# Kernel optimization log

Measured on AMD Instinct MI355X. Metric: run time of the kernel, lower is better.

Reference implementation:

```python
import jax, jax.numpy as jnp
import numpy as np

B, C, H, W = 4, 256, 64, 64
C8 = C // 8


def setup_inputs() -> dict:
    key = jax.random.key(0)
    ks = jax.random.split(key, 8)
    x = jax.random.normal(ks[0], (B, C, H, W), dtype=jnp.float32)
    # 1x1 conv weights act as per-pixel linear maps: [out_ch, in_ch]
    Wq = jax.random.normal(ks[1], (C8, C), dtype=jnp.float32) * 0.05
    bq = jax.random.normal(ks[2], (C8,), dtype=jnp.float32) * 0.01
    Wk = jax.random.normal(ks[3], (C8, C), dtype=jnp.float32) * 0.05
    bk = jax.random.normal(ks[4], (C8,), dtype=jnp.float32) * 0.01
    Wv = jax.random.normal(ks[5], (C, C), dtype=jnp.float32) * 0.05
    bv = jax.random.normal(ks[6], (C,), dtype=jnp.float32) * 0.01
    # torch inits gamma to 0 (identity); use nonzero so output exercises the attention path
    gamma = jnp.array(0.5, dtype=jnp.float32)
    return {"x": x, "Wq": Wq, "bq": bq, "Wk": Wk, "bk": bk, "Wv": Wv, "bv": bv, "gamma": gamma}


def reference(x, Wq, bq, Wk, bk, Wv, bv, gamma):
    b, c, h, w = x.shape
    n = h * w
    xf = x.reshape(b, c, n)                                   # [B,C,N]
    q = jnp.einsum('oc,bcn->bno', Wq, xf) + bq                # [B,N,C8] (proj_query permuted)
    k = jnp.einsum('oc,bcn->bon', Wk, xf) + bk[:, None]       # [B,C8,N]
    energy = jnp.einsum('bnc,bcm->bnm', q, k)                 # [B,N_q,N_k]
    # NOTE: torch Softmax(dim=1) -> normalize over the QUERY axis (axis=1)
    attention = jax.nn.softmax(energy, axis=1)
    v = jnp.einsum('oc,bcn->bon', Wv, xf) + bv[:, None]       # [B,C,N]
    out = jnp.einsum('bcn,bnm->bcm', v, attention).reshape(b, c, h, w)
    return gamma * out + x
```

## Files before the change

kernel.cpp:

```cpp
#include <hip/hip_runtime.h>
#include <hip/hip_bf16.h>

#define BN 4
#define CC 256
#define C8 32
#define NN 4096
#define PROJ_ROWS 320
#define LOG2E 1.4426950408889634f

typedef __attribute__((ext_vector_type(8))) short short8;
typedef __attribute__((ext_vector_type(4))) float f32x4;

__device__ __forceinline__ unsigned short f2bf(float f) {
    unsigned u = __builtin_bit_cast(unsigned, f);
    unsigned r = (u + 0x7fffu + ((u >> 16) & 1u)) >> 16;
    return (unsigned short)r;
}
__device__ __forceinline__ float bfhi2f(unsigned u) { return __builtin_bit_cast(float, u & 0xffff0000u); }
__device__ __forceinline__ float bflo2f(unsigned u) { return __builtin_bit_cast(float, u << 16); }

__global__ __launch_bounds__(256) void proj_kernel(
    const float* __restrict__ x,
    const float* __restrict__ Wq, const float* __restrict__ bq,
    const float* __restrict__ Wk, const float* __restrict__ bk,
    const float* __restrict__ Wv, const float* __restrict__ bv,
    unsigned short* __restrict__ proj, unsigned short* __restrict__ qT)
{
    int bid = blockIdx.x;
    int b = bid >> 7, nt = bid & 127;
    int n0 = nt * 32;
    int tid = threadIdx.x;
    int w = tid >> 6, l = tid & 63, l15 = l & 15, lq = l >> 4;

    __shared__ alignas(16) unsigned short Xt[32][264];

    int c_l = tid >> 3;
    int nb  = (tid & 7) * 4;

#pragma unroll
    for (int kc = 0; kc < 8; kc++) {
        const float* xp = x + ((size_t)(b * CC + kc * 32 + c_l)) * NN + n0 + nb;
        float4 x0 = *(const float4*)xp;
        Xt[nb + 0][kc * 32 + c_l] = f2bf(x0.x);
        Xt[nb + 1][kc * 32 + c_l] = f2bf(x0.y);
        Xt[nb + 2][kc * 32 + c_l] = f2bf(x0.z);
        Xt[nb + 3][kc * 32 + c_l] = f2bf(x0.w);
    }
    __syncthreads();

    f32x4 acc[5][2];
#pragma unroll
    for (int gi = 0; gi < 5; gi++)
#pragma unroll
        for (int mi = 0; mi < 2; mi++) acc[gi][mi] = (f32x4){0.f, 0.f, 0.f, 0.f};

    for (int kc = 0; kc < 8; kc++) {
        float4 wf[5][2];
#pragma unroll
        for (int gi = 0; gi < 5; gi++) {
            int og = (w * 5 + gi) * 16 + l15;
            const float* wrow = (og < 32) ? (Wq + (size_t)og * CC)
                              : (og < 64) ? (Wk + (size_t)(og - 32) * CC)
                                          : (Wv + (size_t)(og - 64) * CC);
            const float* wp = wrow + kc * 32 + lq * 8;
            wf[gi][0] = *(const float4*)wp;
            wf[gi][1] = *(const float4*)(wp + 4);
        }
#pragma unroll
        for (int gi = 0; gi < 5; gi++) {
            unsigned short a8[8] __attribute__((aligned(16)));
            float tw[8] = {wf[gi][0].x, wf[gi][0].y, wf[gi][0].z, wf[gi][0].w,
                           wf[gi][1].x, wf[gi][1].y, wf[gi][1].z, wf[gi][1].w};
#pragma unroll
            for (int e = 0; e < 8; e++) a8[e] = f2bf(tw[e]);
            short8 af = *(const short8*)a8;
#pragma unroll
            for (int mi = 0; mi < 2; mi++) {
                short8 bf = *(const short8*)&Xt[mi * 16 + l15][kc * 32 + lq * 8];
                acc[gi][mi] = __builtin_amdgcn_mfma_f32_16x16x32_bf16(af, bf, acc[gi][mi], 0, 0, 0);
            }
        }
    }

#pragma unroll
    for (int gi = 0; gi < 5; gi++) {
#pragma unroll
        for (int r = 0; r < 4; r++) {
            int og = (w * 5 + gi) * 16 + lq * 4 + r;
            float bias = (og < 32) ? bq[og] : (og < 64) ? bk[og - 32] : bv[og - 64];
            bool is_k = (og >= 32) && (og < 64);
#pragma unroll
            for (int mi = 0; mi < 2; mi++) {
                int n = n0 + mi * 16 + l15;
                float v = acc[gi][mi][r] + bias;
                if (is_k) v *= LOG2E;
                unsigned short v16 = f2bf(v);
                if (og < 32) {
                    qT[((size_t)b * NN + n) * C8 + og] = v16;
                } else {
                    proj[((size_t)b * PROJ_ROWS + og) * NN + n] = v16;
                }
            }
        }
    }
}

template<int NSPLIT, bool FINAL>
__global__ __launch_bounds__(256, 4) void attn_kernel(
    const unsigned short* __restrict__ proj,
    const unsigned short* __restrict__ qT,
    const float* __restrict__ x,
    const float* __restrict__ gamma_p,
    float* __restrict__ out,
    unsigned short* __restrict__ Opart,
    float* __restrict__ Lpart)
{
    constexpr int ITERS = 64 / NSPLIT;
    int bid = blockIdx.x;
    int low = bid & 255;
    int xcd = low & 7;
    int b = xcd >> 1;
    int mtile = ((low >> 3) << 1) | (xcd & 1);
    int m0 = mtile * 64;
    int ch = (bid >> 8) & 1;
    int h  = bid >> 9;
    int nbase = h * (ITERS * 64);

    int tid = threadIdx.x;
    int w = tid >> 6, l = tid & 63, l15 = l & 15, lq = l >> 4;
    int cw = ch * 128 + w * 32;

    __shared__ alignas(16) unsigned short ps[2][64][72];
    __shared__ float red[4][64];
    __shared__ float Ltot[64];

    const unsigned short* kbase = proj + ((size_t)b * PROJ_ROWS + C8) * NN;
    const unsigned short* vbase = proj + ((size_t)b * PROJ_ROWS + 64) * NN;
    const unsigned short* qbase = qT + (size_t)b * NN * C8;

    short8 kfrag[4];
#pragma unroll
    for (int mi = 0; mi < 4; mi++) {
        int col = m0 + mi * 16 + l15;
        unsigned short t8[8] __attribute__((aligned(16)));
#pragma unroll
        for (int j = 0; j < 8; j++)
            t8[j] = kbase[(size_t)(lq * 8 + j) * NN + col];
        kfrag[mi] = *(const short8*)t8;
    }

    f32x4 O[2][4];
#pragma unroll
    for (int ci = 0; ci < 2; ci++)
#pragma unroll
        for (int mi = 0; mi < 4; mi++) O[ci][mi] = (f32x4){0.f, 0.f, 0.f, 0.f};
    float runS[4] = {0.f, 0.f, 0.f, 0.f};

    short8 avc[2][2];
#pragma unroll
    for (int kh = 0; kh < 2; kh++)
#pragma unroll
        for (int ci = 0; ci < 2; ci++)
            avc[kh][ci] = *(const short8*)(vbase
                + (size_t)(cw + ci * 16 + l15) * NN + nbase + kh * 32 + lq * 8);
    {
        short8 qf = *(const short8*)(qbase + (size_t)(nbase + 16 * w + l15) * C8 + lq * 8);
#pragma unroll
        for (int mi = 0; mi < 4; mi++) {
            f32x4 S = __builtin_amdgcn_mfma_f32_16x16x32_bf16(
                qf, kfrag[mi], (f32x4){0.f, 0.f, 0.f, 0.f}, 0, 0, 0);
            float p0 = exp2f(S[0]), p1 = exp2f(S[1]), p2 = exp2f(S[2]), p3 = exp2f(S[3]);
            runS[mi] += (p0 + p1) + (p2 + p3);
            unsigned pk0 = (unsigned)f2bf(p0) | ((unsigned)f2bf(p1) << 16);
            unsigned pk1 = (unsigned)f2bf(p2) | ((unsigned)f2bf(p3) << 16);
            *(uint2*)&ps[0][mi * 16 + l15][16 * w + lq * 4] = make_uint2(pk0, pk1);
        }
    }

    for (int it = 0; it < ITERS; it++) {
        int n0c = nbase + it * 64;
        __syncthreads();

        short8 avn[2][2];
        short8 qn;
        if (it + 1 < ITERS) {
            int nn = n0c + 64;
#pragma unroll
            for (int kh = 0; kh < 2; kh++)
#pragma unroll
                for (int ci = 0; ci < 2; ci++)
                    avn[kh][ci] = *(const short8*)(vbase
                        + (size_t)(cw + ci * 16 + l15) * NN + nn + kh * 32 + lq * 8);
            qn = *(const short8*)(qbase + (size_t)(nn + 16 * w + l15) * C8 + lq * 8);
        }

        const unsigned short* psrc = &ps[it & 1][0][0];
#pragma unroll
        for (int kh = 0; kh < 2; kh++) {
            short8 bfr[4];
#pragma unroll
            for (int mi = 0; mi < 4; mi++)
                bfr[mi] = *(const short8*)(psrc + (mi * 16 + l15) * 72 + kh * 32 + lq * 8);
#pragma unroll
            for (int ci = 0; ci < 2; ci++)
#pragma unroll
                for (int mi = 0; mi < 4; mi++)
                    O[ci][mi] = __builtin_amdgcn_mfma_f32_16x16x32_bf16(
                        avc[kh][ci], bfr[mi], O[ci][mi], 0, 0, 0);
        }

        if (it + 1 < ITERS) {
#pragma unroll
            for (int mi = 0; mi < 4; mi++) {
                f32x4 S = __builtin_amdgcn_mfma_f32_16x16x32_bf16(
                    qn, kfrag[mi], (f32x4){0.f, 0.f, 0.f, 0.f}, 0, 0, 0);
                float p0 = exp2f(S[0]), p1 = exp2f(S[1]), p2 = exp2f(S[2]), p3 = exp2f(S[3]);
                runS[mi] += (p0 + p1) + (p2 + p3);
                unsigned pk0 = (unsigned)f2bf(p0) | ((unsigned)f2bf(p1) << 16);
                unsigned pk1 = (unsigned)f2bf(p2) | ((unsigned)f2bf(p3) << 16);
                *(uint2*)(&ps[(it + 1) & 1][0][0] + (mi * 16 + l15) * 72 + 16 * w + lq * 4)
                    = make_uint2(pk0, pk1);
            }
#pragma unroll
            for (int kh = 0; kh < 2; kh++)
#pragma unroll
                for (int ci = 0; ci < 2; ci++) avc[kh][ci] = avn[kh][ci];
        }
    }

#pragma unroll
    for (int mi = 0; mi < 4; mi++) {
        float s = runS[mi];
        s += __shfl_xor(s, 16);
        s += __shfl_xor(s, 32);
        red[w][mi * 16 + l15] = s;
    }
    __syncthreads();
    if (tid < 64) Ltot[tid] = red[0][tid] + red[1][tid] + red[2][tid] + red[3][tid];
    __syncthreads();

    if constexpr (FINAL) {
        float gamma = gamma_p[0];
        float iv[4];
#pragma unroll
        for (int mi = 0; mi < 4; mi++) iv[mi] = 1.0f / Ltot[mi * 16 + l15];
#pragma unroll
        for (int ci = 0; ci < 2; ci++) {
#pragma unroll
            for (int mi = 0; mi < 4; mi++) {
                int m = m0 + mi * 16 + l15;
#pragma unroll
                for (int r = 0; r < 4; r++) {
                    int c = cw + ci * 16 + lq * 4 + r;
                    size_t idx = ((size_t)b * CC + c) * NN + m;
                    out[idx] = gamma * (O[ci][mi][r] * iv[mi]) + x[idx];
                }
            }
        }
    } else {
        size_t p = ((size_t)h * BN + b) * 64 + mtile;
        if (ch == 0 && tid < 64) Lpart[p * 64 + tid] = Ltot[tid];
        unsigned short* Ob = Opart + p * (size_t)(64 * 256);
#pragma unroll
        for (int ci = 0; ci < 2; ci++) {
#pragma unroll
            for (int mi = 0; mi < 4; mi++) {
                unsigned pk0 = (unsigned)f2bf(O[ci][mi][0]) | ((unsigned)f2bf(O[ci][mi][1]) << 16);
                unsigned pk1 = (unsigned)f2bf(O[ci][mi][2]) | ((unsigned)f2bf(O[ci][mi][3]) << 16);
                *(uint2*)(Ob + (size_t)(mi * 16 + l15) * 256 + cw + ci * 16 + lq * 4)
                    = make_uint2(pk0, pk1);
            }
        }
    }
}

template<int NSPLIT>
__global__ __launch_bounds__(256) void combine_kernel(
    const unsigned short* __restrict__ Opart, const float* __restrict__ Lpart,
    const float* __restrict__ x, const float* __restrict__ gamma_p,
    float* __restrict__ out)
{
    int bid = blockIdx.x;
    int b = bid >> 6, mt = bid & 63;
    int tid = threadIdx.x;
    float gamma = gamma_p[0];

    __shared__ float trans[64][65];

    int m  = tid >> 2;
    int cg = (tid & 3) * 16;

    float Ls = 0.f;
#pragma unroll
    for (int hh = 0; hh < NSPLIT; hh++)
        Ls += Lpart[(((size_t)hh * BN + b) * 64 + mt) * 64 + m];
    float scale = gamma / Ls;

    for (int cc = 0; cc < 4; cc++) {
        float acc[16];
#pragma unroll
        for (int j = 0; j < 16; j++) acc[j] = 0.f;
#pragma unroll
        for (int hh = 0; hh < NSPLIT; hh++) {
            const unsigned short* row = Opart
                + (((size_t)hh * BN + b) * 64 + mt) * (size_t)(64 * 256)
                + (size_t)m * 256 + cc * 64 + cg;
#pragma unroll
            for (int j4 = 0; j4 < 4; j4++) {
                uint2 u = *(const uint2*)(row + j4 * 4);
                acc[j4 * 4 + 0] += bflo2f(u.x);
                acc[j4 * 4 + 1] += bfhi2f(u.x);
                acc[j4 * 4 + 2] += bflo2f(u.y);
                acc[j4 * 4 + 3] += bfhi2f(u.y);
            }
        }
        if (cc) __syncthreads();
#pragma unroll
        for (int j = 0; j < 16; j++) trans[cg + j][m] = acc[j] * scale;
        __syncthreads();

        int c  = tid >> 2;
        int mg = (tid & 3) * 16;
        size_t idx = ((size_t)b * CC + cc * 64 + c) * NN + mt * 64 + mg;
#pragma unroll
        for (int j4 = 0; j4 < 4; j4++) {
            f32x4 xv = *(const f32x4*)(x + idx + j4 * 4);
            f32x4 o;
#pragma unroll
            for (int j = 0; j < 4; j++) o[j] = trans[c][mg + j4 * 4 + j] + xv[j];
            *(f32x4*)(out + idx + j4 * 4) = o;
        }
    }
}

extern "C" void kernel_launch(void* const* d_in, const int* in_sizes, int n_in,
                              void* d_out, int out_size, void* d_ws, size_t ws_size,
                              hipStream_t stream) {
    const float* x     = (const float*)d_in[0];
    const float* Wq    = (const float*)d_in[1];
    const float* bq    = (const float*)d_in[2];
    const float* Wk    = (const float*)d_in[3];
    const float* bk    = (const float*)d_in[4];
    const float* Wv    = (const float*)d_in[5];
    const float* bv    = (const float*)d_in[6];
    const float* gamma = (const float*)d_in[7];
    float* out = (float*)d_out;
    (void)in_sizes; (void)n_in; (void)out_size;

    unsigned short* proj = (unsigned short*)d_ws;
    unsigned short* qT   = proj + (size_t)BN * PROJ_ROWS * NN;
    const size_t baseB = ((size_t)BN * PROJ_ROWS * NN + (size_t)BN * NN * C8) * 2;

    auto needB = [&](size_t ns) {
        size_t LpB = ns * BN * 64 * 64 * 4;
        size_t OpB = ns * BN * 64 * (size_t)(64 * 256) * 2;
        return baseB + LpB + OpB;
    };

    proj_kernel<<<512, 256, 0, stream>>>(x, Wq, bq, Wk, bk, Wv, bv, proj, qT);

    if (ws_size >= needB(4)) {
        float* Lpart = (float*)((char*)d_ws + baseB);
        unsigned short* Opart = (unsigned short*)(Lpart + (size_t)4 * BN * 64 * 64);
        attn_kernel<4, false><<<2048, 256, 0, stream>>>(proj, qT, x, gamma, out, Opart, Lpart);
        combine_kernel<4><<<256, 256, 0, stream>>>(Opart, Lpart, x, gamma, out);
    } else if (ws_size >= needB(2)) {
        float* Lpart = (float*)((char*)d_ws + baseB);
        unsigned short* Opart = (unsigned short*)(Lpart + (size_t)2 * BN * 64 * 64);
        attn_kernel<2, false><<<1024, 256, 0, stream>>>(proj, qT, x, gamma, out, Opart, Lpart);
        combine_kernel<2><<<256, 256, 0, stream>>>(Opart, Lpart, x, gamma, out);
    } else {
        attn_kernel<1, true><<<512, 256, 0, stream>>>(proj, qT, x, gamma, out, nullptr, nullptr);
    }
}
```

Measured before the change: 188.5 us.

## Pre-cast weights to bf16, use hardware exp2/pack cvt, split combine across channels

```diff
diff --git a/kernel.cpp b/kernel.cpp
--- a/kernel.cpp
+++ b/kernel.cpp
@@ -16,14 +16,34 @@
     unsigned r = (u + 0x7fffu + ((u >> 16) & 1u)) >> 16;
     return (unsigned short)r;
 }
+__device__ __forceinline__ unsigned pk2bf(float a, float b) {
+#if __has_builtin(__builtin_amdgcn_cvt_pk_bf16_f32)
+    auto v = __builtin_amdgcn_cvt_pk_bf16_f32(a, b);
+    return __builtin_bit_cast(unsigned, v);
+#else
+    return (unsigned)f2bf(a) | ((unsigned)f2bf(b) << 16);
+#endif
+}
 __device__ __forceinline__ float bfhi2f(unsigned u) { return __builtin_bit_cast(float, u & 0xffff0000u); }
 __device__ __forceinline__ float bflo2f(unsigned u) { return __builtin_bit_cast(float, u << 16); }
 
+__global__ __launch_bounds__(256) void wcast_kernel(
+    const float* __restrict__ Wq, const float* __restrict__ Wk,
+    const float* __restrict__ Wv, unsigned short* __restrict__ Wbf)
+{
+    int o = blockIdx.x, c = threadIdx.x;
+    float v;
+    if (o < 32)      v = Wq[(size_t)o * CC + c];
+    else if (o < 64) v = Wk[(size_t)(o - 32) * CC + c] * LOG2E;
+    else             v = Wv[(size_t)(o - 64) * CC + c];
+    Wbf[(size_t)o * CC + c] = f2bf(v);
+}
+
 __global__ __launch_bounds__(256) void proj_kernel(
     const float* __restrict__ x,
-    const float* __restrict__ Wq, const float* __restrict__ bq,
-    const float* __restrict__ Wk, const float* __restrict__ bk,
-    const float* __restrict__ Wv, const float* __restrict__ bv,
+    const unsigned short* __restrict__ Wbf,
+    const float* __restrict__ bq, const float* __restrict__ bk,
+    const float* __restrict__ bv,
     unsigned short* __restrict__ proj, unsigned short* __restrict__ qT)
 {
     int bid = blockIdx.x;
@@ -55,29 +75,18 @@
         for (int mi = 0; mi < 2; mi++) acc[gi][mi] = (f32x4){0.f, 0.f, 0.f, 0.f};
 
     for (int kc = 0; kc < 8; kc++) {
-        float4 wf[5][2];
+        short8 af[5];
 #pragma unroll
         for (int gi = 0; gi < 5; gi++) {
             int og = (w * 5 + gi) * 16 + l15;
-            const float* wrow = (og < 32) ? (Wq + (size_t)og * CC)
-                              : (og < 64) ? (Wk + (size_t)(og - 32) * CC)
-                                          : (Wv + (size_t)(og - 64) * CC);
-            const float* wp = wrow + kc * 32 + lq * 8;
-            wf[gi][0] = *(const float4*)wp;
-            wf[gi][1] = *(const float4*)(wp + 4);
+            af[gi] = *(const short8*)(Wbf + (size_t)og * CC + kc * 32 + lq * 8);
         }
 #pragma unroll
         for (int gi = 0; gi < 5; gi++) {
-            unsigned short a8[8] __attribute__((aligned(16)));
-            float tw[8] = {wf[gi][0].x, wf[gi][0].y, wf[gi][0].z, wf[gi][0].w,
-                           wf[gi][1].x, wf[gi][1].y, wf[gi][1].z, wf[gi][1].w};
-#pragma unroll
-            for (int e = 0; e < 8; e++) a8[e] = f2bf(tw[e]);
-            short8 af = *(const short8*)a8;
 #pragma unroll
             for (int mi = 0; mi < 2; mi++) {
                 short8 bf = *(const short8*)&Xt[mi * 16 + l15][kc * 32 + lq * 8];
-                acc[gi][mi] = __builtin_amdgcn_mfma_f32_16x16x32_bf16(af, bf, acc[gi][mi], 0, 0, 0);
+                acc[gi][mi] = __builtin_amdgcn_mfma_f32_16x16x32_bf16(af[gi], bf, acc[gi][mi], 0, 0, 0);
             }
         }
     }
@@ -87,14 +96,13 @@
 #pragma unroll
         for (int r = 0; r < 4; r++) {
             int og = (w * 5 + gi) * 16 + lq * 4 + r;
-            float bias = (og < 32) ? bq[og] : (og < 64) ? bk[og - 32] : bv[og - 64];
-            bool is_k = (og >= 32) && (og < 64);
+            float bias = (og < 32) ? bq[og]
+                       : (og < 64) ? bk[og - 32] * LOG2E
+                                   : bv[og - 64];
 #pragma unroll
             for (int mi = 0; mi < 2; mi++) {
                 int n = n0 + mi * 16 + l15;
-                float v = acc[gi][mi][r] + bias;
-                if (is_k) v *= LOG2E;
-                unsigned short v16 = f2bf(v);
+                unsigned short v16 = f2bf(acc[gi][mi][r] + bias);
                 if (og < 32) {
                     qT[((size_t)b * NN + n) * C8 + og] = v16;
                 } else {
@@ -154,7 +162,9 @@
     for (int ci = 0; ci < 2; ci++)
 #pragma unroll
         for (int mi = 0; mi < 4; mi++) O[ci][mi] = (f32x4){0.f, 0.f, 0.f, 0.f};
-    float runS[4] = {0.f, 0.f, 0.f, 0.f};
+    f32x4 runS[4];
+#pragma unroll
+    for (int mi = 0; mi < 4; mi++) runS[mi] = (f32x4){0.f, 0.f, 0.f, 0.f};
 
     short8 avc[2][2];
 #pragma unroll
@@ -169,11 +179,12 @@
         for (int mi = 0; mi < 4; mi++) {
             f32x4 S = __builtin_amdgcn_mfma_f32_16x16x32_bf16(
                 qf, kfrag[mi], (f32x4){0.f, 0.f, 0.f, 0.f}, 0, 0, 0);
-            float p0 = exp2f(S[0]), p1 = exp2f(S[1]), p2 = exp2f(S[2]), p3 = exp2f(S[3]);
-            runS[mi] += (p0 + p1) + (p2 + p3);
-            unsigned pk0 = (unsigned)f2bf(p0) | ((unsigned)f2bf(p1) << 16);
-            unsigned pk1 = (unsigned)f2bf(p2) | ((unsigned)f2bf(p3) << 16);
-            *(uint2*)&ps[0][mi * 16 + l15][16 * w + lq * 4] = make_uint2(pk0, pk1);
+            f32x4 P;
+#pragma unroll
+            for (int j = 0; j < 4; j++) P[j] = __builtin_amdgcn_exp2f(S[j]);
+            runS[mi] += P;
+            *(uint2*)&ps[0][mi * 16 + l15][16 * w + lq * 4]
+                = make_uint2(pk2bf(P[0], P[1]), pk2bf(P[2], P[3]));
         }
     }
 
@@ -214,12 +225,12 @@
             for (int mi = 0; mi < 4; mi++) {
                 f32x4 S = __builtin_amdgcn_mfma_f32_16x16x32_bf16(
                     qn, kfrag[mi], (f32x4){0.f, 0.f, 0.f, 0.f}, 0, 0, 0);
-                float p0 = exp2f(S[0]), p1 = exp2f(S[1]), p2 = exp2f(S[2]), p3 = exp2f(S[3]);
-                runS[mi] += (p0 + p1) + (p2 + p3);
-                unsigned pk0 = (unsigned)f2bf(p0) | ((unsigned)f2bf(p1) << 16);
-                unsigned pk1 = (unsigned)f2bf(p2) | ((unsigned)f2bf(p3) << 16);
+                f32x4 P;
+#pragma unroll
+                for (int j = 0; j < 4; j++) P[j] = __builtin_amdgcn_exp2f(S[j]);
+                runS[mi] += P;
                 *(uint2*)(&ps[(it + 1) & 1][0][0] + (mi * 16 + l15) * 72 + 16 * w + lq * 4)
-                    = make_uint2(pk0, pk1);
+                    = make_uint2(pk2bf(P[0], P[1]), pk2bf(P[2], P[3]));
             }
 #pragma unroll
             for (int kh = 0; kh < 2; kh++)
@@ -230,7 +241,7 @@
 
 #pragma unroll
     for (int mi = 0; mi < 4; mi++) {
-        float s = runS[mi];
+        float s = (runS[mi][0] + runS[mi][1]) + (runS[mi][2] + runS[mi][3]);
         s += __shfl_xor(s, 16);
         s += __shfl_xor(s, 32);
         red[w][mi * 16 + l15] = s;
@@ -265,10 +276,9 @@
         for (int ci = 0; ci < 2; ci++) {
 #pragma unroll
             for (int mi = 0; mi < 4; mi++) {
-                unsigned pk0 = (unsigned)f2bf(O[ci][mi][0]) | ((unsigned)f2bf(O[ci][mi][1]) << 16);
-                unsigned pk1 = (unsigned)f2bf(O[ci][mi][2]) | ((unsigned)f2bf(O[ci][mi][3]) << 16);
                 *(uint2*)(Ob + (size_t)(mi * 16 + l15) * 256 + cw + ci * 16 + lq * 4)
-                    = make_uint2(pk0, pk1);
+                    = make_uint2(pk2bf(O[ci][mi][0], O[ci][mi][1]),
+                                 pk2bf(O[ci][mi][2], O[ci][mi][3]));
             }
         }
     }
@@ -281,7 +291,9 @@
     float* __restrict__ out)
 {
     int bid = blockIdx.x;
-    int b = bid >> 6, mt = bid & 63;
+    int cq = bid & 3;
+    int mt = (bid >> 2) & 63;
+    int b  = bid >> 8;
     int tid = threadIdx.x;
     float gamma = gamma_p[0];
 
@@ -296,40 +308,37 @@
         Ls += Lpart[(((size_t)hh * BN + b) * 64 + mt) * 64 + m];
     float scale = gamma / Ls;
 
-    for (int cc = 0; cc < 4; cc++) {
-        float acc[16];
-#pragma unroll
-        for (int j = 0; j < 16; j++) acc[j] = 0.f;
-#pragma unroll
-        for (int hh = 0; hh < NSPLIT; hh++) {
-            const unsigned short* row = Opart
-                + (((size_t)hh * BN + b) * 64 + mt) * (size_t)(64 * 256)
-                + (size_t)m * 256 + cc * 64 + cg;
-#pragma unroll
-            for (int j4 = 0; j4 < 4; j4++) {
-                uint2 u = *(const uint2*)(row + j4 * 4);
-                acc[j4 * 4 + 0] += bflo2f(u.x);
-                acc[j4 * 4 + 1] += bfhi2f(u.x);
-                acc[j4 * 4 + 2] += bflo2f(u.y);
-                acc[j4 * 4 + 3] += bfhi2f(u.y);
-            }
-        }
-        if (cc) __syncthreads();
-#pragma unroll
-        for (int j = 0; j < 16; j++) trans[cg + j][m] = acc[j] * scale;
-        __syncthreads();
-
-        int c  = tid >> 2;
-        int mg = (tid & 3) * 16;
-        size_t idx = ((size_t)b * CC + cc * 64 + c) * NN + mt * 64 + mg;
+    float acc[16];
+#pragma unroll
+    for (int j = 0; j < 16; j++) acc[j] = 0.f;
+#pragma unroll
+    for (int hh = 0; hh < NSPLIT; hh++) {
+        const unsigned short* row = Opart
+            + (((size_t)hh * BN + b) * 64 + mt) * (size_t)(64 * 256)
+            + (size_t)m * 256 + cq * 64 + cg;
 #pragma unroll
         for (int j4 = 0; j4 < 4; j4++) {
-            f32x4 xv = *(const f32x4*)(x + idx + j4 * 4);
-            f32x4 o;
-#pragma unroll
-            for (int j = 0; j < 4; j++) o[j] = trans[c][mg + j4 * 4 + j] + xv[j];
-            *(f32x4*)(out + idx + j4 * 4) = o;
-        }
+            uint2 u = *(const uint2*)(row + j4 * 4);
+            acc[j4 * 4 + 0] += bflo2f(u.x);
+            acc[j4 * 4 + 1] += bfhi2f(u.x);
+            acc[j4 * 4 + 2] += bflo2f(u.y);
+            acc[j4 * 4 + 3] += bfhi2f(u.y);
+        }
+    }
+#pragma unroll
+    for (int j = 0; j < 16; j++) trans[cg + j][m] = acc[j] * scale;
+    __syncthreads();
+
+    int c  = tid >> 2;
+    int mg = (tid & 3) * 16;
+    size_t idx = ((size_t)b * CC + cq * 64 + c) * NN + mt * 64 + mg;
+#pragma unroll
+    for (int j4 = 0; j4 < 4; j4++) {
+        f32x4 xv = *(const f32x4*)(x + idx + j4 * 4);
+        f32x4 o;
+#pragma unroll
+        for (int j = 0; j < 4; j++) o[j] = trans[c][mg + j4 * 4 + j] + xv[j];
+        *(f32x4*)(out + idx + j4 * 4) = o;
     }
 }
 
@@ -349,7 +358,10 @@
 
     unsigned short* proj = (unsigned short*)d_ws;
     unsigned short* qT   = proj + (size_t)BN * PROJ_ROWS * NN;
-    const size_t baseB = ((size_t)BN * PROJ_ROWS * NN + (size_t)BN * NN * C8) * 2;
+    unsigned short* Wbf  = qT + (size_t)BN * NN * C8;
+    const size_t baseB = ((size_t)BN * PROJ_ROWS * NN
+                        + (size_t)BN * NN * C8
+                        + (size_t)PROJ_ROWS * CC) * 2;
 
     auto needB = [&](size_t ns) {
         size_t LpB = ns * BN * 64 * 64 * 4;
@@ -357,18 +369,19 @@
         return baseB + LpB + OpB;
     };
 
-    proj_kernel<<<512, 256, 0, stream>>>(x, Wq, bq, Wk, bk, Wv, bv, proj, qT);
+    wcast_kernel<<<320, 256, 0, stream>>>(Wq, Wk, Wv, Wbf);
+    proj_kernel<<<512, 256, 0, stream>>>(x, Wbf, bq, bk, bv, proj, qT);
 
     if (ws_size >= needB(4)) {
         float* Lpart = (float*)((char*)d_ws + baseB);
         unsigned short* Opart = (unsigned short*)(Lpart + (size_t)4 * BN * 64 * 64);
         attn_kernel<4, false><<<2048, 256, 0, stream>>>(proj, qT, x, gamma, out, Opart, Lpart);
-        combine_kernel<4><<<256, 256, 0, stream>>>(Opart, Lpart, x, gamma, out);
+        combine_kernel<4><<<1024, 256, 0, stream>>>(Opart, Lpart, x, gamma, out);
     } else if (ws_size >= needB(2)) {
         float* Lpart = (float*)((char*)d_ws + baseB);
         unsigned short* Opart = (unsigned short*)(Lpart + (size_t)2 * BN * 64 * 64);
         attn_kernel<2, false><<<1024, 256, 0, stream>>>(proj, qT, x, gamma, out, Opart, Lpart);
-        combine_kernel<2><<<256, 256, 0, stream>>>(Opart, Lpart, x, gamma, out);
+        combine_kernel<2><<<1024, 256, 0, stream>>>(Opart, Lpart, x, gamma, out);
     } else {
         attn_kernel<1, true><<<512, 256, 0, stream>>>(proj, qT, x, gamma, out, nullptr, nullptr);
     }
```

Measured after the change: 183.3 us. 2.8% less time.
